# Optimization experiments

Hardware: AMD Instinct MI355X
Metric: run time of the kernel (lower is better)

## Reference

```python
import jax, jax.numpy as jnp
import numpy as np

B, N, D, E, A, DIAM = 16, 1024, 128, 16384, 64, 3


def setup_inputs() -> dict:
    key = jax.random.key(0)
    ks = jax.random.split(key, 20)
    s = 0.05
    inp = {
        "node_features": jax.random.normal(ks[0], (B, N, D), jnp.float32),
        "edge_features": jax.random.normal(ks[1], (B, N, N), jnp.float32),
        "src_idx": jax.random.randint(ks[2], (E,), 0, N, jnp.int32),
        "tgt_idx": jax.random.randint(ks[3], (E,), 0, N, jnp.int32),
        # message MLP: Linear(2D+1 -> D)
        "W_msg": jax.random.normal(ks[4], (2 * D + 1, D), jnp.float32) * s,
        "b_msg": jax.random.normal(ks[5], (D,), jnp.float32) * s,
        # GRUCell(D, D), gate order r,z,n (torch convention)
        "W_ih": jax.random.normal(ks[6], (3 * D, D), jnp.float32) * s,
        "W_hh": jax.random.normal(ks[7], (3 * D, D), jnp.float32) * s,
        "b_ih": jax.random.normal(ks[8], (3 * D,), jnp.float32) * s,
        "b_hh": jax.random.normal(ks[9], (3 * D,), jnp.float32) * s,
        # readout: Linear(D,D)+SELU, Linear(D,D)+SELU, then policy head Linear(D,A)
        "W_r1": jax.random.normal(ks[10], (D, D), jnp.float32) * s,
        "b_r1": jax.random.normal(ks[11], (D,), jnp.float32) * s,
        "W_r2": jax.random.normal(ks[12], (D, D), jnp.float32) * s,
        "b_r2": jax.random.normal(ks[13], (D,), jnp.float32) * s,
        "W_pol": jax.random.normal(ks[14], (D, A), jnp.float32) * s,
        "b_pol": jax.random.normal(ks[15], (A,), jnp.float32) * s,
    }
    return inp


def reference(node_features, edge_features, src_idx, tgt_idx,
              W_msg, b_msg, W_ih, W_hh, b_ih, b_hh,
              W_r1, b_r1, W_r2, b_r2, W_pol, b_pol):
    h = node_features  # [B, N, D]
    ef = edge_features[:, src_idx, tgt_idx][..., None]  # [B, E, 1], constant across rounds
    for _ in range(DIAM):
        src_f = h[:, src_idx]  # [B, E, D] gather
        tgt_f = h[:, tgt_idx]  # [B, E, D]
        comb = jnp.concatenate([src_f, tgt_f, ef], axis=-1)  # [B, E, 2D+1]
        msg = jax.nn.selu(comb @ W_msg + b_msg)  # [B, E, D]
        # scatter-sum messages onto target nodes
        agg = jax.vmap(lambda m: jax.ops.segment_sum(m, tgt_idx, num_segments=N))(msg)  # [B, N, D]
        # GRUCell update (torch math, gate order r,z,n; b_hn stays inside r*(...))
        gi = agg @ W_ih.T + b_ih  # [B, N, 3D]
        gh = h @ W_hh.T + b_hh    # [B, N, 3D]
        i_r, i_z, i_n = jnp.split(gi, 3, axis=-1)
        h_r, h_z, h_n = jnp.split(gh, 3, axis=-1)
        r = jax.nn.sigmoid(i_r + h_r)
        z = jax.nn.sigmoid(i_z + h_z)
        n = jnp.tanh(i_n + r * h_n)
        h = (1.0 - z) * n + z * h
    pooled = h.sum(axis=1)  # [B, D]
    pooled = jax.nn.selu(pooled @ W_r1 + b_r1)
    pooled = jax.nn.selu(pooled @ W_r2 + b_r2)
    return pooled @ W_pol + b_pol  # [B, A] policy logits
```

## Files before the change

### kernel.cpp

```cpp
#include <hip/hip_runtime.h>
#include <hip/hip_bf16.h>
#include <math.h>

constexpr int kB = 16;
constexpr int kN = 1024;
constexpr int kD = 128;
constexpr int kE = 16384;

typedef short bf16x8 __attribute__((ext_vector_type(8)));
typedef float f32x4 __attribute__((ext_vector_type(4)));
typedef unsigned short us4 __attribute__((ext_vector_type(4)));

__device__ __forceinline__ float selu_f(float x) {
    const float scale = 1.0507009873554805f;
    const float alpha = 1.6732632423543772f;
    return x > 0.f ? scale * x : scale * alpha * (expf(x) - 1.f);
}

__device__ __forceinline__ float sigmoid_f(float x) {
    return 1.f / (1.f + expf(-x));
}

__device__ __forceinline__ float bf2f(unsigned short u) {
    union { unsigned int i; float f; } x;
    x.i = ((unsigned int)u) << 16;
    return x.f;
}

__device__ __forceinline__ unsigned short f2bf(float f) {
    union { float f; unsigned int i; } u;
    u.f = f;
    const unsigned int r = u.i + 0x7fffu + ((u.i >> 16) & 1u);
    return (unsigned short)(r >> 16);
}

__global__ void k_h0c(const float* __restrict__ nodef, unsigned short* __restrict__ h_bf,
                      const int* __restrict__ tgt, int* __restrict__ cnt) {
    int gid = blockIdx.x * 256 + threadIdx.x;
    h_bf[gid] = f2bf(nodef[gid]);
    if (gid < kE) atomicAdd(&cnt[tgt[gid]], 1);
}

__global__ void k_scan(const int* __restrict__ cnt, int* __restrict__ cursor,
                       int* __restrict__ rowstart) {
    __shared__ int s[kN];
    int t = threadIdx.x;
    int own = cnt[t];
    s[t] = own;
    __syncthreads();
    for (int off = 1; off < kN; off <<= 1) {
        int add = (t >= off) ? s[t - off] : 0;
        __syncthreads();
        s[t] += add;
        __syncthreads();
    }
    int excl = s[t] - own;
    cursor[t] = excl;
    rowstart[t] = excl;
    if (t == kN - 1) rowstart[kN] = s[t];
}

__global__ void k_scatter(const int* __restrict__ src, const int* __restrict__ tgt,
                          int* __restrict__ cursor, int* __restrict__ sid,
                          int* __restrict__ ssrc) {
    int e = blockIdx.x * 256 + threadIdx.x;
    int tg = tgt[e];
    int pos = atomicAdd(&cursor[tg], 1);
    sid[pos] = e;
    ssrc[pos] = src[e];
}

__global__ void k_gather_ef(const float* __restrict__ edgef, const int* __restrict__ src,
                            const int* __restrict__ tgt, const int* __restrict__ sid,
                            float* __restrict__ efg) {
    int gid = blockIdx.x * 256 + threadIdx.x;
    int b = gid >> 14;
    int i = gid & (kE - 1);
    int eid = sid[i];
    efg[gid] = edgef[(size_t)b * kN * kN + (size_t)src[eid] * kN + tgt[eid]];
}

__global__ void k_buildw(const float* __restrict__ Wmsg, const float* __restrict__ Whh,
                         const float* __restrict__ Wih,
                         const float* __restrict__ bih, const float* __restrict__ bhh,
                         unsigned short* __restrict__ WcatT,
                         unsigned short* __restrict__ Wfused,
                         float* __restrict__ bihP, float* __restrict__ bhhP) {
    const int j = blockIdx.x;
    const int k = threadIdx.x;
    if (j < 256) {
        float v = (j < 128) ? Wmsg[k * 128 + j] : Wmsg[(128 + k) * 128 + (j - 128)];
        WcatT[j * 128 + k] = f2bf(v);
    } else {
        const int f = j - 256;
        const int dg = f / 48, rem = f % 48;
        const int g = rem / 16, di = rem % 16;
        const int orig = g * 128 + dg * 16 + di;
        Wfused[(size_t)f * 256 + k] = f2bf(Wih[(size_t)orig * 128 + k]);
        Wfused[(size_t)f * 256 + 128 + k] = f2bf(Whh[(size_t)orig * 128 + k]);
        if (k == 0) {
            bihP[f] = bih[orig];
            bhhP[f] = bhh[orig];
        }
    }
}

__launch_bounds__(256)
__global__ void k_mm256(const unsigned short* __restrict__ A,
                        const unsigned short* __restrict__ Bt,
                        unsigned short* __restrict__ HST) {
    __shared__ uint4 As[2048];
    __shared__ uint4 Bs[2048];
    const int t = threadIdx.x;
    const int r0 = blockIdx.x * 128;
    const int c0 = blockIdx.y * 128;
    const uint4* gA = (const uint4*)(A + (size_t)r0 * 128);
    const uint4* gB = (const uint4*)(Bt + (size_t)c0 * 128);
#pragma unroll
    for (int i = 0; i < 8; ++i) {
        const int f = i * 256 + t;
        const int row = f >> 4, c16 = f & 15;
        const int d = row * 16 + (c16 ^ (row & 7));
        As[d] = gA[f];
        Bs[d] = gB[f];
    }
    __syncthreads();
    const int w = t >> 6, l = t & 63;
    const int wm = (w & 1) * 64, wn = (w >> 1) * 64;
    const int lin = l & 15, kq = l >> 4;
    f32x4 acc[4][4] = {};
#pragma unroll
    for (int s = 0; s < 4; ++s) {
        bf16x8 a[4], b[4];
#pragma unroll
        for (int mi = 0; mi < 4; ++mi) {
            const int row = wm + mi * 16 + lin;
            a[mi] = *(const bf16x8*)&As[row * 16 + ((s * 4 + kq) ^ (row & 7))];
        }
#pragma unroll
        for (int ni = 0; ni < 4; ++ni) {
            const int row = wn + ni * 16 + lin;
            b[ni] = *(const bf16x8*)&Bs[row * 16 + ((s * 4 + kq) ^ (row & 7))];
        }
#pragma unroll
        for (int mi = 0; mi < 4; ++mi)
#pragma unroll
            for (int ni = 0; ni < 4; ++ni)
                acc[mi][ni] = __builtin_amdgcn_mfma_f32_16x16x32_bf16(
                    a[mi], b[ni], acc[mi][ni], 0, 0, 0);
    }
    const int rq = kq * 4;
#pragma unroll
    for (int ni = 0; ni < 4; ++ni) {
        const int col = c0 + wn + ni * 16 + lin;
#pragma unroll
        for (int mi = 0; mi < 4; ++mi) {
            const int row = r0 + wm + mi * 16 + rq;
#pragma unroll
            for (int r = 0; r < 4; ++r)
                HST[(size_t)(row + r) * 256 + col] = f2bf(acc[mi][ni][r]);
        }
    }
}

__launch_bounds__(256)
__global__ void k_edge(const unsigned short* __restrict__ HST, const float* __restrict__ efg,
                       const int* __restrict__ ssrc, const int* __restrict__ rowstart,
                       const float* __restrict__ Wmsg, const float* __restrict__ bmsg,
                       unsigned short* __restrict__ agg_bf) {
    __shared__ float4 part[2][4][32];
    const int t = threadIdx.x;
    const int b = blockIdx.y;
    const int tl = t >> 7;
    const int tg = blockIdx.x * 2 + tl;
    const int slot = (t >> 5) & 3;
    const int lane = t & 31;
    const int c = lane * 4;
    const float4 w3 = *(const float4*)&Wmsg[256 * 128 + c];
    const float4 bm = *(const float4*)&bmsg[c];
    const size_t base = (size_t)b * kN;
    const us4 htu = *(const us4*)&HST[(base + tg) * 256 + 128 + c];
    const float hb0 = bf2f(htu.x) + bm.x;
    const float hb1 = bf2f(htu.y) + bm.y;
    const float hb2 = bf2f(htu.z) + bm.z;
    const float hb3 = bf2f(htu.w) + bm.w;
    const float* efb = efg + b * kE;
    const int j0 = rowstart[tg], j1 = rowstart[tg + 1];
    float a0 = 0.f, a1 = 0.f, a2 = 0.f, a3 = 0.f;
    for (int j = j0 + slot; j < j1; j += 4) {
        const int s = ssrc[j];
        const float ef = efb[j];
        const us4 hs = *(const us4*)&HST[(base + s) * 256 + c];
        a0 += selu_f(bf2f(hs.x) + fmaf(ef, w3.x, hb0));
        a1 += selu_f(bf2f(hs.y) + fmaf(ef, w3.y, hb1));
        a2 += selu_f(bf2f(hs.z) + fmaf(ef, w3.z, hb2));
        a3 += selu_f(bf2f(hs.w) + fmaf(ef, w3.w, hb3));
    }
    part[tl][slot][lane] = make_float4(a0, a1, a2, a3);
    __syncthreads();
    if (slot == 0) {
        const float4 p1 = part[tl][1][lane];
        const float4 p2 = part[tl][2][lane];
        const float4 p3 = part[tl][3][lane];
        a0 += p1.x + p2.x + p3.x;
        a1 += p1.y + p2.y + p3.y;
        a2 += p1.z + p2.z + p3.z;
        a3 += p1.w + p2.w + p3.w;
        us4 o;
        o.x = f2bf(a0);
        o.y = f2bf(a1);
        o.z = f2bf(a2);
        o.w = f2bf(a3);
        *(us4*)&agg_bf[(base + tg) * 128 + c] = o;
    }
}

__launch_bounds__(256)
__global__ void k_gigru(const unsigned short* __restrict__ agg_bf,
                        const unsigned short* __restrict__ h_bf_in,
                        const unsigned short* __restrict__ Wfused,
                        const float* __restrict__ bihP, const float* __restrict__ bhhP,
                        unsigned short* __restrict__ h_bf_out,
                        float* __restrict__ pooled, int lastIter) {
    __shared__ uint4 As[2048];
    __shared__ uint4 Bs[1536];
    const int t = threadIdx.x;
    const int r0 = blockIdx.x * 128;
    const int y = blockIdx.y;
    const int w = t >> 6, l = t & 63;
    const int wm = (w & 1) * 64, wc0 = (w >> 1) * 48;
    const int lin = l & 15, kq = l >> 4, rq = kq * 4;
    f32x4 acc[4][3] = {};
    f32x4 accN[4] = {};
#pragma unroll
    for (int stage = 0; stage < 2; ++stage) {
        const unsigned short* Ap = stage ? h_bf_in : agg_bf;
        const uint4* gA = (const uint4*)(Ap + (size_t)r0 * 128);
#pragma unroll
        for (int i = 0; i < 8; ++i) {
            const int f = i * 256 + t;
            const int row = f >> 4, c16 = f & 15;
            As[row * 16 + (c16 ^ (row & 7))] = gA[f];
        }
        const uint4* gW = (const uint4*)Wfused;
#pragma unroll
        for (int i = 0; i < 6; ++i) {
            const int f = i * 256 + t;
            const int j = f >> 4, c16 = f & 15;
            Bs[j * 16 + (c16 ^ (j & 7))] = gW[(size_t)(y * 96 + j) * 32 + stage * 16 + c16];
        }
        __syncthreads();
#pragma unroll
        for (int ks = 0; ks < 4; ++ks) {
            bf16x8 a[4], b[3];
#pragma unroll
            for (int mi = 0; mi < 4; ++mi) {
                const int row = wm + mi * 16 + lin;
                a[mi] = *(const bf16x8*)&As[row * 16 + ((ks * 4 + kq) ^ (row & 7))];
            }
#pragma unroll
            for (int ni = 0; ni < 3; ++ni) {
                const int row = wc0 + ni * 16 + lin;
                b[ni] = *(const bf16x8*)&Bs[row * 16 + ((ks * 4 + kq) ^ (row & 7))];
            }
#pragma unroll
            for (int mi = 0; mi < 4; ++mi) {
                acc[mi][0] = __builtin_amdgcn_mfma_f32_16x16x32_bf16(a[mi], b[0], acc[mi][0], 0, 0, 0);
                acc[mi][1] = __builtin_amdgcn_mfma_f32_16x16x32_bf16(a[mi], b[1], acc[mi][1], 0, 0, 0);
                if (stage == 0)
                    acc[mi][2] = __builtin_amdgcn_mfma_f32_16x16x32_bf16(a[mi], b[2], acc[mi][2], 0, 0, 0);
                else
                    accN[mi] = __builtin_amdgcn_mfma_f32_16x16x32_bf16(a[mi], b[2], accN[mi], 0, 0, 0);
            }
        }
        __syncthreads();
    }
    const int colR = y * 96 + wc0 + lin;
    const float bR = bihP[colR] + bhhP[colR];
    const float bZ = bihP[colR + 16] + bhhP[colR + 16];
    const float biN = bihP[colR + 32];
    const float bhN = bhhP[colR + 32];
    const int dgg = y * 2 + (wc0 / 48);
    const int d = dgg * 16 + lin;
    const int bb = r0 >> 10;
    const int dc = d >> 3, de = d & 7;
    float psum = 0.f;
#pragma unroll
    for (int mi = 0; mi < 4; ++mi) {
#pragma unroll
        for (int r = 0; r < 4; ++r) {
            const int rowL = wm + mi * 16 + rq + r;
            const float rr = sigmoid_f(acc[mi][0][r] + bR);
            const float zz = sigmoid_f(acc[mi][1][r] + bZ);
            const float i_n = acc[mi][2][r] + biN;
            const float h_n = accN[mi][r] + bhN;
            const float nn = tanhf(fmaf(rr, h_n, i_n));
            const float hv = bf2f(((const unsigned short*)&As[rowL * 16 + (dc ^ (rowL & 7))])[de]);
            const float o = fmaf(zz, hv - nn, nn);
            h_bf_out[(size_t)(r0 + rowL) * 128 + d] = f2bf(o);
            psum += o;
        }
    }
    if (lastIter) atomicAdd(&pooled[bb * 128 + d], psum);
}

__global__ void k_head(const float* __restrict__ pooled,
                       const float* __restrict__ Wr1, const float* __restrict__ br1,
                       const float* __restrict__ Wr2, const float* __restrict__ br2,
                       const float* __restrict__ Wpol, const float* __restrict__ bpol,
                       float* __restrict__ out) {
    __shared__ float p[128], t1[128];
    const int b = blockIdx.x, d = threadIdx.x;
    p[d] = pooled[b * 128 + d];
    __syncthreads();
    float acc = br1[d];
    for (int k = 0; k < 128; ++k) acc = fmaf(p[k], Wr1[k * 128 + d], acc);
    t1[d] = selu_f(acc);
    __syncthreads();
    acc = br2[d];
    for (int k = 0; k < 128; ++k) acc = fmaf(t1[k], Wr2[k * 128 + d], acc);
    __syncthreads();
    p[d] = selu_f(acc);
    __syncthreads();
    if (d < 64) {
        float o = bpol[d];
        for (int k = 0; k < 128; ++k) o = fmaf(p[k], Wpol[k * 64 + d], o);
        out[b * 64 + d] = o;
    }
}

extern "C" void kernel_launch(void* const* d_in, const int* in_sizes, int n_in,
                              void* d_out, int out_size, void* d_ws, size_t ws_size,
                              hipStream_t stream) {
    const float* nodef = (const float*)d_in[0];
    const float* edgef = (const float*)d_in[1];
    const int* src = (const int*)d_in[2];
    const int* tgt = (const int*)d_in[3];
    const float* Wmsg = (const float*)d_in[4];
    const float* bmsg = (const float*)d_in[5];
    const float* Wih = (const float*)d_in[6];
    const float* Whh = (const float*)d_in[7];
    const float* bih = (const float*)d_in[8];
    const float* bhh = (const float*)d_in[9];
    const float* Wr1 = (const float*)d_in[10];
    const float* br1 = (const float*)d_in[11];
    const float* Wr2 = (const float*)d_in[12];
    const float* br2 = (const float*)d_in[13];
    const float* Wpol = (const float*)d_in[14];
    const float* bpol = (const float*)d_in[15];
    float* out = (float*)d_out;

    float* ws = (float*)d_ws;
    float* efg = ws;
    float* bihP = efg + 262144;
    float* bhhP = bihP + 384;
    int* cnt = (int*)(bhhP + 384);
    float* pooled = (float*)(cnt + 1024);
    unsigned short* HST = (unsigned short*)(pooled + 2048);
    unsigned short* hbfA = HST + 4194304;
    unsigned short* hbfB = hbfA + 2097152;
    unsigned short* agg_bf = hbfB + 2097152;
    unsigned short* WcatT = agg_bf + 2097152;
    unsigned short* Wfused = WcatT + 32768;
    int* cursor = (int*)(Wfused + 98304);
    int* rowstart = cursor + 1024;
    int* sid = rowstart + 1040;
    int* ssrc = sid + 16384;

    hipMemsetAsync(cnt, 0, (1024 + 2048) * sizeof(int), stream);
    k_h0c<<<(kB * kN * kD) / 256, 256, 0, stream>>>(nodef, hbfA, tgt, cnt);
    k_scan<<<1, 1024, 0, stream>>>(cnt, cursor, rowstart);
    k_scatter<<<kE / 256, 256, 0, stream>>>(src, tgt, cursor, sid, ssrc);
    k_gather_ef<<<(kB * kE) / 256, 256, 0, stream>>>(edgef, src, tgt, sid, efg);
    k_buildw<<<640, 128, 0, stream>>>(Wmsg, Whh, Wih, bih, bhh, WcatT, Wfused, bihP, bhhP);

    for (int it = 0; it < 3; ++it) {
        unsigned short* hcur = (it & 1) ? hbfB : hbfA;
        unsigned short* hnxt = (it & 1) ? hbfA : hbfB;
        k_mm256<<<dim3(128, 2), 256, 0, stream>>>(hcur, WcatT, HST);
        k_edge<<<dim3(kN / 2, kB), 256, 0, stream>>>(HST, efg, ssrc, rowstart, Wmsg, bmsg, agg_bf);
        k_gigru<<<dim3(128, 4), 256, 0, stream>>>(agg_bf, hcur, Wfused, bihP, bhhP, hnxt,
                                                  pooled, it == 2 ? 1 : 0);
    }

    k_head<<<kB, 128, 0, stream>>>(pooled, Wr1, br1, Wr2, br2, Wpol, bpol, out);
}
```

Baseline: 304.1 us.

## Fuse preprocessing kernels, vectorize HST stores, use fast transcendentals

Merges the bf16 conversion, edge counting and weight-building kernels into one launch, and merges scan and scatter into a single-block kernel using LDS atomics. Gather of edge features now reads sorted src/tgt directly instead of going through an edge-id indirection. The GEMM swaps MFMA operands so each lane holds 4 consecutive columns, allowing packed 8-byte stores of HST. Sigmoid/tanh/selu switch to __expf and hardware reciprocal, trading a little accuracy for fewer instructions.

```diff
diff --git a/kernel.cpp b/kernel.cpp
--- a/kernel.cpp
+++ b/kernel.cpp
@@ -14,11 +14,15 @@
 __device__ __forceinline__ float selu_f(float x) {
     const float scale = 1.0507009873554805f;
     const float alpha = 1.6732632423543772f;
-    return x > 0.f ? scale * x : scale * alpha * (expf(x) - 1.f);
+    return x > 0.f ? scale * x : scale * alpha * (__expf(x) - 1.f);
 }
 
 __device__ __forceinline__ float sigmoid_f(float x) {
-    return 1.f / (1.f + expf(-x));
+    return __builtin_amdgcn_rcpf(1.f + __expf(-x));
+}
+
+__device__ __forceinline__ float tanh_f(float x) {
+    return 1.f - 2.f * __builtin_amdgcn_rcpf(1.f + __expf(2.f * x));
 }
 
 __device__ __forceinline__ float bf2f(unsigned short u) {
@@ -34,18 +38,55 @@
     return (unsigned short)(r >> 16);
 }
 
-__global__ void k_h0c(const float* __restrict__ nodef, unsigned short* __restrict__ h_bf,
-                      const int* __restrict__ tgt, int* __restrict__ cnt) {
-    int gid = blockIdx.x * 256 + threadIdx.x;
-    h_bf[gid] = f2bf(nodef[gid]);
-    if (gid < kE) atomicAdd(&cnt[tgt[gid]], 1);
-}
-
-__global__ void k_scan(const int* __restrict__ cnt, int* __restrict__ cursor,
-                       int* __restrict__ rowstart) {
+__global__ void k_h0cw(const float* __restrict__ nodef, unsigned short* __restrict__ h_bf,
+                       const int* __restrict__ tgt, int* __restrict__ cnt,
+                       const float* __restrict__ Wmsg, const float* __restrict__ Whh,
+                       const float* __restrict__ Wih,
+                       const float* __restrict__ bih, const float* __restrict__ bhh,
+                       unsigned short* __restrict__ WcatT,
+                       unsigned short* __restrict__ Wfused,
+                       float* __restrict__ bihP, float* __restrict__ bhhP) {
+    const int bid = blockIdx.x;
+    const int t = threadIdx.x;
+    if (bid < 2048) {
+        const int gid = bid * 256 + t;
+        const float4 v = ((const float4*)nodef)[gid];
+        us4 o;
+        o.x = f2bf(v.x);
+        o.y = f2bf(v.y);
+        o.z = f2bf(v.z);
+        o.w = f2bf(v.w);
+        ((us4*)h_bf)[gid] = o;
+        if (gid < kE) atomicAdd(&cnt[tgt[gid]], 1);
+    } else {
+        const int j = (bid - 2048) * 2 + (t >> 7);
+        const int k = t & 127;
+        if (j < 256) {
+            float v = (j < 128) ? Wmsg[k * 128 + j] : Wmsg[(128 + k) * 128 + (j - 128)];
+            WcatT[j * 128 + k] = f2bf(v);
+        } else {
+            const int f = j - 256;
+            const int dg = f / 48, rem = f % 48;
+            const int g = rem / 16, di = rem % 16;
+            const int orig = g * 128 + dg * 16 + di;
+            Wfused[(size_t)f * 256 + k] = f2bf(Wih[(size_t)orig * 128 + k]);
+            Wfused[(size_t)f * 256 + 128 + k] = f2bf(Whh[(size_t)orig * 128 + k]);
+            if (k == 0) {
+                bihP[f] = bih[orig];
+                bhhP[f] = bhh[orig];
+            }
+        }
+    }
+}
+
+__launch_bounds__(1024)
+__global__ void k_scansct(const int* __restrict__ cnt, const int* __restrict__ src,
+                          const int* __restrict__ tgt, int* __restrict__ rowstart,
+                          int* __restrict__ ssrc, int* __restrict__ stgt) {
     __shared__ int s[kN];
-    int t = threadIdx.x;
-    int own = cnt[t];
+    __shared__ int cur[kN];
+    const int t = threadIdx.x;
+    const int own = cnt[t];
     s[t] = own;
     __syncthreads();
     for (int off = 1; off < kN; off <<= 1) {
@@ -54,55 +95,25 @@
         s[t] += add;
         __syncthreads();
     }
-    int excl = s[t] - own;
-    cursor[t] = excl;
+    const int excl = s[t] - own;
+    cur[t] = excl;
     rowstart[t] = excl;
     if (t == kN - 1) rowstart[kN] = s[t];
-}
-
-__global__ void k_scatter(const int* __restrict__ src, const int* __restrict__ tgt,
-                          int* __restrict__ cursor, int* __restrict__ sid,
-                          int* __restrict__ ssrc) {
-    int e = blockIdx.x * 256 + threadIdx.x;
-    int tg = tgt[e];
-    int pos = atomicAdd(&cursor[tg], 1);
-    sid[pos] = e;
-    ssrc[pos] = src[e];
-}
-
-__global__ void k_gather_ef(const float* __restrict__ edgef, const int* __restrict__ src,
-                            const int* __restrict__ tgt, const int* __restrict__ sid,
-                            float* __restrict__ efg) {
-    int gid = blockIdx.x * 256 + threadIdx.x;
-    int b = gid >> 14;
-    int i = gid & (kE - 1);
-    int eid = sid[i];
-    efg[gid] = edgef[(size_t)b * kN * kN + (size_t)src[eid] * kN + tgt[eid]];
-}
-
-__global__ void k_buildw(const float* __restrict__ Wmsg, const float* __restrict__ Whh,
-                         const float* __restrict__ Wih,
-                         const float* __restrict__ bih, const float* __restrict__ bhh,
-                         unsigned short* __restrict__ WcatT,
-                         unsigned short* __restrict__ Wfused,
-                         float* __restrict__ bihP, float* __restrict__ bhhP) {
-    const int j = blockIdx.x;
-    const int k = threadIdx.x;
-    if (j < 256) {
-        float v = (j < 128) ? Wmsg[k * 128 + j] : Wmsg[(128 + k) * 128 + (j - 128)];
-        WcatT[j * 128 + k] = f2bf(v);
-    } else {
-        const int f = j - 256;
-        const int dg = f / 48, rem = f % 48;
-        const int g = rem / 16, di = rem % 16;
-        const int orig = g * 128 + dg * 16 + di;
-        Wfused[(size_t)f * 256 + k] = f2bf(Wih[(size_t)orig * 128 + k]);
-        Wfused[(size_t)f * 256 + 128 + k] = f2bf(Whh[(size_t)orig * 128 + k]);
-        if (k == 0) {
-            bihP[f] = bih[orig];
-            bhhP[f] = bhh[orig];
-        }
-    }
+    __syncthreads();
+    for (int e = t; e < kE; e += 1024) {
+        const int tg = tgt[e];
+        const int pos = atomicAdd(&cur[tg], 1);
+        ssrc[pos] = src[e];
+        stgt[pos] = tg;
+    }
+}
+
+__global__ void k_gather_ef(const float* __restrict__ edgef, const int* __restrict__ ssrc,
+                            const int* __restrict__ stgt, float* __restrict__ efg) {
+    const int gid = blockIdx.x * 256 + threadIdx.x;
+    const int b = gid >> 14;
+    const int i = gid & (kE - 1);
+    efg[gid] = edgef[(size_t)b * kN * kN + (size_t)ssrc[i] * kN + stgt[i]];
 }
 
 __launch_bounds__(256)
@@ -147,18 +158,21 @@
 #pragma unroll
             for (int ni = 0; ni < 4; ++ni)
                 acc[mi][ni] = __builtin_amdgcn_mfma_f32_16x16x32_bf16(
-                    a[mi], b[ni], acc[mi][ni], 0, 0, 0);
+                    b[ni], a[mi], acc[mi][ni], 0, 0, 0);
     }
     const int rq = kq * 4;
 #pragma unroll
-    for (int ni = 0; ni < 4; ++ni) {
-        const int col = c0 + wn + ni * 16 + lin;
-#pragma unroll
-        for (int mi = 0; mi < 4; ++mi) {
-            const int row = r0 + wm + mi * 16 + rq;
-#pragma unroll
-            for (int r = 0; r < 4; ++r)
-                HST[(size_t)(row + r) * 256 + col] = f2bf(acc[mi][ni][r]);
+    for (int mi = 0; mi < 4; ++mi) {
+        const int row = r0 + wm + mi * 16 + lin;
+#pragma unroll
+        for (int ni = 0; ni < 4; ++ni) {
+            const int col = c0 + wn + ni * 16 + rq;
+            us4 o;
+            o.x = f2bf(acc[mi][ni][0]);
+            o.y = f2bf(acc[mi][ni][1]);
+            o.z = f2bf(acc[mi][ni][2]);
+            o.w = f2bf(acc[mi][ni][3]);
+            *(us4*)&HST[(size_t)row * 256 + col] = o;
         }
     }
 }
@@ -294,7 +308,7 @@
             const float zz = sigmoid_f(acc[mi][1][r] + bZ);
             const float i_n = acc[mi][2][r] + biN;
             const float h_n = accN[mi][r] + bhN;
-            const float nn = tanhf(fmaf(rr, h_n, i_n));
+            const float nn = tanh_f(fmaf(rr, h_n, i_n));
             const float hv = bf2f(((const unsigned short*)&As[rowL * 16 + (dc ^ (rowL & 7))])[de]);
             const float o = fmaf(zz, hv - nn, nn);
             h_bf_out[(size_t)(r0 + rowL) * 128 + d] = f2bf(o);
@@ -362,17 +376,15 @@
     unsigned short* agg_bf = hbfB + 2097152;
     unsigned short* WcatT = agg_bf + 2097152;
     unsigned short* Wfused = WcatT + 32768;
-    int* cursor = (int*)(Wfused + 98304);
-    int* rowstart = cursor + 1024;
-    int* sid = rowstart + 1040;
-    int* ssrc = sid + 16384;
+    int* stgt = (int*)(Wfused + 98304);
+    int* rowstart = stgt + 16384;
+    int* ssrc = rowstart + 1040;
 
     hipMemsetAsync(cnt, 0, (1024 + 2048) * sizeof(int), stream);
-    k_h0c<<<(kB * kN * kD) / 256, 256, 0, stream>>>(nodef, hbfA, tgt, cnt);
-    k_scan<<<1, 1024, 0, stream>>>(cnt, cursor, rowstart);
-    k_scatter<<<kE / 256, 256, 0, stream>>>(src, tgt, cursor, sid, ssrc);
-    k_gather_ef<<<(kB * kE) / 256, 256, 0, stream>>>(edgef, src, tgt, sid, efg);
-    k_buildw<<<640, 128, 0, stream>>>(Wmsg, Whh, Wih, bih, bhh, WcatT, Wfused, bihP, bhhP);
+    k_h0cw<<<2048 + 320, 256, 0, stream>>>(nodef, hbfA, tgt, cnt, Wmsg, Whh, Wih, bih, bhh,
+                                           WcatT, Wfused, bihP, bhhP);
+    k_scansct<<<1, 1024, 0, stream>>>(cnt, src, tgt, rowstart, ssrc, stgt);
+    k_gather_ef<<<(kB * kE) / 256, 256, 0, stream>>>(edgef, ssrc, stgt, efg);
 
     for (int it = 0; it < 3; ++it) {
         unsigned short* hcur = (it & 1) ? hbfB : hbfA;
```

New measurement: 303.3 us. Within noise of the previous version (-0.3%).
